# Performance work log

Hardware: AMD Instinct MI355X
Metric: run time of the kernel (lower is better)

Reference implementation:

```python
import jax, jax.numpy as jnp
import numpy as np

E = 1024   # n_embd
H = 16     # n_heads
D = 64     # head_dim
G = 4      # n_kv_groups
F = 4096   # ffn hidden_dim
V = 32000  # vocab
L = 4      # n_layers (all full_attention)
B = 1
T = 2048
ROT = 16   # partial_rotary_factor 0.25 * head_dim 64, rounded to even
EPS = 1e-6
THETA = 10000.0


def rope_tables(seq_len):
    # matches compute_rope_params: inv_freq over even indices of rotary_dim
    inv_freq = 1.0 / (THETA ** (jnp.arange(0, ROT, 2, dtype=jnp.float32) / ROT))
    ang = jnp.arange(seq_len, dtype=jnp.float32)[:, None] * inv_freq[None, :]
    ang = jnp.concatenate([ang, ang], axis=1)  # [T, ROT]
    return jnp.cos(ang), jnp.sin(ang)


def rmsnorm(x, w):
    # torch RMSNorm: x * rsqrt(mean(x^2)+eps) * (1 + weight)
    xf = x.astype(jnp.float32)
    n = xf * jax.lax.rsqrt(jnp.mean(xf * xf, axis=-1, keepdims=True) + EPS)
    return (n * (1.0 + w)).astype(x.dtype)


def apply_rope(x, cos, sin):
    # x: [B, h, T, D]; cos/sin: [1, 1, T, ROT]; partial rotary on first ROT dims
    x_rot, x_pass = x[..., :ROT], x[..., ROT:]
    x1, x2 = x_rot[..., :ROT // 2], x_rot[..., ROT // 2:]
    rotated = jnp.concatenate([-x2, x1], axis=-1)
    return jnp.concatenate([x_rot * cos + rotated * sin, x_pass], axis=-1)


def _forward(tokens, emb, Wq, Wk, Wv, Wo, qn, kn, n1, n2, f1, f2, f3, fn, head):
    cos, sin = rope_tables(T)
    cos = cos[None, None]  # [1,1,T,ROT]
    sin = sin[None, None]
    mask = jnp.triu(jnp.ones((T, T), dtype=bool), k=1)  # True = masked
    scale = D ** -0.5
    x = emb[tokens]  # [B,T,E]

    def block(x, p):
        wq, wk, wv, wo, qw, kw, w1, w2, g1, g2, g3 = p
        h = rmsnorm(x, w1)
        # fused Q + gate projection -> [B,T,H,2D], chunk on last dim
        qg = (h @ wq).reshape(B, T, H, 2 * D)
        q = qg[..., :D].transpose(0, 2, 1, 3)            # [B,H,T,D]
        gate = qg[..., D:].reshape(B, T, H * D)          # [B,T,H*D]
        k = (h @ wk).reshape(B, T, G, D).transpose(0, 2, 1, 3)  # [B,G,T,D]
        v = (h @ wv).reshape(B, T, G, D).transpose(0, 2, 1, 3)
        q = rmsnorm(q, qw)
        k = rmsnorm(k, kw)
        q = apply_rope(q, cos, sin)
        k = apply_rope(k, cos, sin)
        k = jnp.repeat(k, H // G, axis=1)  # GQA expand -> [B,H,T,D]
        v = jnp.repeat(v, H // G, axis=1)
        scores = jnp.einsum('bhqd,bhkd->bhqk', q, k)
        scores = jnp.where(mask, -jnp.inf, scores) * scale
        w = jax.nn.softmax(scores.astype(jnp.float32), axis=-1).astype(q.dtype)
        ctx = jnp.einsum('bhqk,bhkd->bhqd', w, v)
        ctx = ctx.transpose(0, 2, 1, 3).reshape(B, T, H * D)
        ctx = ctx * jax.nn.sigmoid(gate)
        x = x + ctx @ wo
        h2 = rmsnorm(x, w2)
        ff = (jax.nn.silu(h2 @ g1) * (h2 @ g2)) @ g3
        return x + ff, None

    params = (Wq, Wk, Wv, Wo, qn, kn, n1, n2, f1, f2, f3)
    x, _ = jax.lax.scan(block, x, params)
    return rmsnorm(x, fn) @ head  # logits [B,T,V]


def setup_inputs() -> dict:
    key = jax.random.key(0)
    ks = jax.random.split(key, 16)
    s = 0.02
    rn = lambda k, shape, sc=s: jax.random.normal(k, shape, jnp.float32) * sc
    return {
        'tokens': jax.random.randint(ks[0], (B, T), 0, V),
        'emb': rn(ks[1], (V, E)),
        'Wq': rn(ks[2], (L, E, 2 * H * D)),
        'Wk': rn(ks[3], (L, E, G * D)),
        'Wv': rn(ks[4], (L, E, G * D)),
        'Wo': rn(ks[5], (L, H * D, E)),
        'qn': rn(ks[6], (L, D)),
        'kn': rn(ks[7], (L, D)),
        'n1': rn(ks[8], (L, E)),
        'n2': rn(ks[9], (L, E)),
        'f1': rn(ks[10], (L, E, F)),
        'f2': rn(ks[11], (L, E, F)),
        'f3': rn(ks[12], (L, F, E)),
        'fn': rn(ks[13], (E,)),
        'head': rn(ks[14], (E, V)),
    }


def reference(tokens, emb, Wq, Wk, Wv, Wo, qn, kn, n1, n2, f1, f2, f3, fn, head):
    return _forward(tokens, emb, Wq, Wk, Wv, Wo, qn, kn, n1, n2, f1, f2, f3, fn, head)
```

## Files before the change

kernel.cpp:

```cpp
#include <hip/hip_runtime.h>

#define T_LEN 2048
#define E_DIM 1024
#define H_N 16
#define G_N 4
#define D_H 64
#define F_DIM 4096
#define V_SZ 32000
#define L_N 4

typedef __attribute__((ext_vector_type(8))) __bf16 bf16x8;
typedef __attribute__((ext_vector_type(4))) float f32x4;

__device__ __forceinline__ unsigned short f2bf(float f){
  unsigned int u = __float_as_uint(f);
  unsigned int r = (u + 0x7FFFu + ((u >> 16) & 1u)) >> 16;
  return (unsigned short)r;
}

__device__ __forceinline__ unsigned int packbf(float a, float b){
  return (unsigned int)f2bf(a) | ((unsigned int)f2bf(b) << 16);
}

__device__ __forceinline__ f32x4 mfma16(bf16x8 a, bf16x8 b, f32x4 c){
  return __builtin_amdgcn_mfma_f32_16x16x32_bf16(a, b, c, 0, 0, 0);
}

__device__ __forceinline__ void gl16(const void* g, void* l){
  __builtin_amdgcn_global_load_lds((const __attribute__((address_space(1))) void*)g,
                                   (__attribute__((address_space(3))) void*)l, 16, 0, 0);
}

#define SBAR() __builtin_amdgcn_s_barrier()
#define LGK0() do{ asm volatile("s_waitcnt lgkmcnt(0)" ::: "memory"); __builtin_amdgcn_sched_barrier(0); }while(0)
#define VMC4() do{ asm volatile("s_waitcnt vmcnt(4)" ::: "memory"); __builtin_amdgcn_sched_barrier(0); }while(0)
#define VMC0() do{ asm volatile("s_waitcnt vmcnt(0)" ::: "memory"); __builtin_amdgcn_sched_barrier(0); }while(0)

#define QSCALE 0.1803368801111183f

__global__ __launch_bounds__(256) void embed_k(const float* __restrict__ emb,
                                               const int* __restrict__ tokens,
                                               float* __restrict__ x){
  int t = blockIdx.x;
  int tok = tokens[t];
  const float4* src = (const float4*)(emb + (size_t)tok * E_DIM);
  float4* dst = (float4*)(x + (size_t)t * E_DIM);
  dst[threadIdx.x] = src[threadIdx.x];
}

__global__ __launch_bounds__(256) void transpose_bf16(const float* __restrict__ src,
                                                      unsigned short* __restrict__ dst,
                                                      int R, int C){
  __shared__ float tile[32][33];
  int c0 = blockIdx.x * 32, r0 = blockIdx.y * 32;
  int tx = threadIdx.x & 31, ty = threadIdx.x >> 5;
  for (int i = 0; i < 4; i++){
    int r = ty + i * 8;
    tile[r][tx] = src[(size_t)(r0 + r) * C + c0 + tx];
  }
  __syncthreads();
  for (int i = 0; i < 4; i++){
    int r = ty + i * 8;
    dst[(size_t)(c0 + r) * R + r0 + tx] = f2bf(tile[tx][r]);
  }
}

__device__ __forceinline__ void tr32(const float* __restrict__ src, unsigned short* __restrict__ dst,
                                     int R, int C, int bx, int by, float* tile ){
  int c0 = bx * 32, r0 = by * 32;
  int tx = threadIdx.x & 31, ty = threadIdx.x >> 5;
  for (int i = 0; i < 4; i++){
    int r = ty + i * 8;
    tile[r * 33 + tx] = src[(size_t)(r0 + r) * C + c0 + tx];
  }
  __syncthreads();
  for (int i = 0; i < 4; i++){
    int r = ty + i * 8;
    dst[(size_t)(c0 + r) * R + r0 + tx] = f2bf(tile[tx * 33 + r]);
  }
}

__global__ __launch_bounds__(256) void prep_weights(const float* __restrict__ Wq, const float* __restrict__ Wk,
                                                    const float* __restrict__ Wv, const float* __restrict__ Wo,
                                                    const float* __restrict__ f1, const float* __restrict__ f2,
                                                    const float* __restrict__ f3,
                                                    unsigned short* __restrict__ wt_qkv,
                                                    unsigned short* __restrict__ wt_o,
                                                    unsigned short* __restrict__ wt_f12i,
                                                    unsigned short* __restrict__ wt_f3){
  __shared__ float sh[1100];
  int id = blockIdx.x;
  if (id < 2048){ tr32(Wq, wt_qkv, 1024, 2048, id & 63, id >> 6, sh); return; }
  id -= 2048;
  if (id < 256){ tr32(Wk, wt_qkv + 2048 * 1024, 1024, 256, id & 7, id >> 3, sh); return; }
  id -= 256;
  if (id < 256){ tr32(Wv, wt_qkv + 2304 * 1024, 1024, 256, id & 7, id >> 3, sh); return; }
  id -= 256;
  if (id < 1024){ tr32(Wo, wt_o, 1024, 1024, id & 31, id >> 5, sh); return; }
  id -= 1024;
  if (id < 4096){ tr32(f3, wt_f3, 4096, 1024, id & 31, id >> 5, sh); return; }
  id -= 4096;
  {
    int q = id & 255, kb = id >> 8;
    float* t1 = sh; float* t2 = sh + 32 * 17;
    int c = threadIdx.x & 15, kk0 = threadIdx.x >> 4;
    for (int p = 0; p < 2; p++){
      int kk = p * 16 + kk0;
      t1[kk * 17 + c] = f1[(size_t)(kb * 32 + kk) * F_DIM + q * 16 + c];
      t2[kk * 17 + c] = f2[(size_t)(kb * 32 + kk) * F_DIM + q * 16 + c];
    }
    __syncthreads();
    int kk = threadIdx.x & 31, rb = threadIdx.x >> 5;
    for (int i = 0; i < 4; i++){
      int r = i * 8 + rb;
      float v = (r < 16) ? t1[kk * 17 + r] : t2[kk * 17 + (r - 16)];
      wt_f12i[(size_t)(q * 32 + r) * 1024 + kb * 32 + kk] = f2bf(v);
    }
  }
}

__global__ __launch_bounds__(256) void rmsnorm_k(const float* __restrict__ x,
                                                 const float* __restrict__ w,
                                                 unsigned short* __restrict__ out){
  const int t = blockIdx.x, tid = threadIdx.x;
  const float4 v = ((const float4*)(x + (size_t)t * E_DIM))[tid];
  float ss = v.x*v.x + v.y*v.y + v.z*v.z + v.w*v.w;
  for (int m = 1; m < 64; m <<= 1) ss += __shfl_xor(ss, m);
  __shared__ float red[4];
  if ((tid & 63) == 0) red[tid >> 6] = ss;
  __syncthreads();
  ss = red[0] + red[1] + red[2] + red[3];
  const float r = rsqrtf(ss * (1.0f / E_DIM) + 1e-6f);
  const float4 wv = ((const float4*)w)[tid];
  ushort4 o;
  o.x = f2bf(v.x * r * (1.0f + wv.x));
  o.y = f2bf(v.y * r * (1.0f + wv.y));
  o.z = f2bf(v.z * r * (1.0f + wv.z));
  o.w = f2bf(v.w * r * (1.0f + wv.w));
  ((ushort4*)(out + (size_t)t * E_DIM))[tid] = o;
}

template<int MODE>
__global__ __launch_bounds__(256) void gemm64_bt(const unsigned short* __restrict__ A,
                                                 const unsigned short* __restrict__ Bt,
                                                 float* __restrict__ C,
                                                 int M, int N, int K){
  __shared__ unsigned short As[64 * 32];
  __shared__ unsigned short Bs[128 * 32];
  const int tid = threadIdx.x;
  const int lane = tid & 63, w = tid >> 6;
  const int l15 = lane & 15, l4 = lane >> 4;

  const int chunk = gridDim.x >> 3;
  const int wgid = (blockIdx.x & 7) * chunk + (blockIdx.x >> 3);
  const int nm = M >> 6;
  const int bm = wgid % nm, bn = wgid / nm;
  const int m0 = bm * 64, n0 = bn * 128;

  const int KS = K / gridDim.y;
  const int kbeg = blockIdx.y * KS;

  const int r0 = tid >> 2;
  const int c0 = (tid & 3) << 3;

  const unsigned short* gA  = A  + (size_t)(m0 + r0) * K + c0;
  const unsigned short* gB0 = Bt + (size_t)(n0 + r0) * K + c0;
  const unsigned short* gB1 = Bt + (size_t)(n0 + 64 + r0) * K + c0;
  unsigned short* lA  = As + w * 512;
  unsigned short* lB0 = Bs + w * 512;
  unsigned short* lB1 = Bs + 2048 + w * 512;

  f32x4 acc[4][2] = {};

  for (int k0 = kbeg; k0 < kbeg + KS; k0 += 32){
    __syncthreads();
    gl16(gA  + k0, lA);
    gl16(gB0 + k0, lB0);
    gl16(gB1 + k0, lB1);
    __syncthreads();
    bf16x8 af[4], bfr[2];
    for (int i = 0; i < 4; i++)
      af[i] = *(const bf16x8*)&As[(i * 16 + l15) * 32 + l4 * 8];
    for (int j = 0; j < 2; j++)
      bfr[j] = *(const bf16x8*)&Bs[(w * 32 + j * 16 + l15) * 32 + l4 * 8];
    for (int i = 0; i < 4; i++)
      for (int j = 0; j < 2; j++)
        acc[i][j] = mfma16(af[i], bfr[j], acc[i][j]);
  }

  for (int i = 0; i < 4; i++)
    for (int j = 0; j < 2; j++){
      int col = n0 + w * 32 + j * 16 + l15;
      for (int r = 0; r < 4; r++){
        int row = m0 + i * 16 + l4 * 4 + r;
        size_t idx = (size_t)row * N + col;
        if (MODE == 0) C[idx] = acc[i][j][r];
        else if (MODE == 1) C[idx] += acc[i][j][r];
        else atomicAdd(&C[idx], acc[i][j][r]);
      }
    }
}

template<int EPI>
__global__ __launch_bounds__(512, 2) void gemm256(const unsigned short* __restrict__ A,
                                                  const unsigned short* __restrict__ Bt,
                                                  float* __restrict__ outF,
                                                  unsigned short* __restrict__ outH,
                                                  int M, int N, int K){
  __shared__ unsigned short lds[65536];
  const int tid = threadIdx.x;
  const int lane = tid & 63, w = tid >> 6;
  const int wm = w >> 2, wn = w & 3;
  const int l15 = lane & 15, l4 = lane >> 4;

  const int nwg = gridDim.x;
  const int xcd = (int)blockIdx.x & 7, lin = (int)blockIdx.x >> 3;
  const int q8 = nwg >> 3, r8 = nwg & 7;
  const int wgid = (xcd < r8 ? xcd * (q8 + 1) : r8 * (q8 + 1) + (xcd - r8) * q8) + lin;
  const int nm = M >> 8;
  const int bm = wgid % nm, bn = wgid / nm;
  const int m0 = bm * 256, n0 = bn * 256;

  const int KS = K / gridDim.y;
  const int kbeg = blockIdx.y * KS;
  const int NT = KS >> 6;

  const int srow = (lane >> 3);
  const int scol = lane & 7;

  auto stageA = [&](int b, int h, int kt){
    #pragma unroll
    for (int c = 0; c < 2; c++){
      int r = w * 16 + c * 8 + srow;
      const unsigned short* g = A + (size_t)(m0 + h * 128 + r) * K + kbeg + kt * 64 + ((scol ^ (r & 7)) << 3);
      gl16(g, (char*)lds + (b * 2 + h) * 16384 + (w * 16 + c * 8) * 128);
    }
  };
  auto stageB = [&](int b, int h, int kt){
    #pragma unroll
    for (int c = 0; c < 2; c++){
      int r = w * 16 + c * 8 + srow;
      const unsigned short* g = Bt + (size_t)(n0 + h * 128 + r) * K + kbeg + kt * 64 + ((scol ^ (r & 7)) << 3);
      gl16(g, (char*)lds + 65536 + (b * 2 + h) * 16384 + (w * 16 + c * 8) * 128);
    }
  };

  const int sl0 = ((l4)     ^ (l15 & 7)) << 4;
  const int sl1 = ((4 | l4) ^ (l15 & 7)) << 4;

  f32x4 acc[8][4] = {};
  bf16x8 aF[8], bF[8];

  stageA(0, 0, 0); stageA(0, 1, 0); stageB(0, 0, 0); stageB(0, 1, 0);
  if (NT > 1){ stageB(1, 0, 1); stageB(1, 1, 1); }
  VMC4();
  SBAR();

  for (int kt = 0; kt < NT; kt++){
    const int buf = kt & 1;
    const char* Ab = (const char*)lds + (buf * 2 + wm) * 16384;
    const char* Bb = (const char*)lds + 65536 + (buf * 2 + (wn >> 1)) * 16384;
    const int brbase = (wn & 1) * 64;

    #pragma unroll
    for (int mf = 0; mf < 4; mf++){
      int r = mf * 16 + l15;
      aF[mf * 2 + 0] = *(const bf16x8*)(Ab + r * 128 + sl0);
      aF[mf * 2 + 1] = *(const bf16x8*)(Ab + r * 128 + sl1);
    }
    #pragma unroll
    for (int nf = 0; nf < 2; nf++){
      int r = brbase + nf * 16 + l15;
      bF[nf * 2 + 0] = *(const bf16x8*)(Bb + r * 128 + sl0);
      bF[nf * 2 + 1] = *(const bf16x8*)(Bb + r * 128 + sl1);
    }
    if (kt + 1 < NT) stageA(buf ^ 1, 0, kt + 1);
    SBAR(); LGK0();
    __builtin_amdgcn_s_setprio(1);
    #pragma unroll
    for (int mf = 0; mf < 4; mf++)
      #pragma unroll
      for (int nf = 0; nf < 2; nf++){
        acc[mf][nf] = mfma16(aF[mf * 2 + 0], bF[nf * 2 + 0], acc[mf][nf]);
        acc[mf][nf] = mfma16(aF[mf * 2 + 1], bF[nf * 2 + 1], acc[mf][nf]);
      }
    __builtin_amdgcn_s_setprio(0);
    SBAR();

    #pragma unroll
    for (int nf = 2; nf < 4; nf++){
      int r = brbase + nf * 16 + l15;
      bF[nf * 2 + 0] = *(const bf16x8*)(Bb + r * 128 + sl0);
      bF[nf * 2 + 1] = *(const bf16x8*)(Bb + r * 128 + sl1);
    }
    if (kt + 1 < NT) stageA(buf ^ 1, 1, kt + 1);
    SBAR(); LGK0();
    __builtin_amdgcn_s_setprio(1);
    #pragma unroll
    for (int mf = 0; mf < 4; mf++)
      #pragma unroll
      for (int nf = 2; nf < 4; nf++){
        acc[mf][nf] = mfma16(aF[mf * 2 + 0], bF[nf * 2 + 0], acc[mf][nf]);
        acc[mf][nf] = mfma16(aF[mf * 2 + 1], bF[nf * 2 + 1], acc[mf][nf]);
      }
    __builtin_amdgcn_s_setprio(0);
    SBAR();

    #pragma unroll
    for (int mf = 0; mf < 4; mf++){
      int r = 64 + mf * 16 + l15;
      aF[mf * 2 + 0] = *(const bf16x8*)(Ab + r * 128 + sl0);
      aF[mf * 2 + 1] = *(const bf16x8*)(Ab + r * 128 + sl1);
    }
    if (kt + 2 < NT) stageB(buf, 0, kt + 2);
    SBAR(); LGK0();
    __builtin_amdgcn_s_setprio(1);
    #pragma unroll
    for (int mf = 0; mf < 4; mf++)
      #pragma unroll
      for (int nf = 2; nf < 4; nf++){
        acc[4 + mf][nf] = mfma16(aF[mf * 2 + 0], bF[nf * 2 + 0], acc[4 + mf][nf]);
        acc[4 + mf][nf] = mfma16(aF[mf * 2 + 1], bF[nf * 2 + 1], acc[4 + mf][nf]);
      }
    __builtin_amdgcn_s_setprio(0);
    SBAR();

    if (kt + 2 < NT) stageB(buf, 1, kt + 2);
    SBAR();
    __builtin_amdgcn_s_setprio(1);
    #pragma unroll
    for (int mf = 0; mf < 4; mf++)
      #pragma unroll
      for (int nf = 0; nf < 2; nf++){
        acc[4 + mf][nf] = mfma16(aF[mf * 2 + 0], bF[nf * 2 + 0], acc[4 + mf][nf]);
        acc[4 + mf][nf] = mfma16(aF[mf * 2 + 1], bF[nf * 2 + 1], acc[4 + mf][nf]);
      }
    __builtin_amdgcn_s_setprio(0);
    if (kt + 2 < NT) { VMC4(); } else { VMC0(); }
    SBAR();
  }

  if (EPI == 0 || EPI == 2){
    #pragma unroll
    for (int mfg = 0; mfg < 8; mfg++){
      #pragma unroll
      for (int nf = 0; nf < 4; nf++){
        int col = n0 + wn * 64 + nf * 16 + l15;
        int row0 = m0 + wm * 128 + mfg * 16 + l4 * 4;
        #pragma unroll
        for (int r = 0; r < 4; r++){
          size_t idx = (size_t)(row0 + r) * N + col;
          if (EPI == 0) outF[idx] = acc[mfg][nf][r];
          else atomicAdd(&outF[idx], acc[mfg][nf][r]);
        }
      }
    }
  } else {
    const int NH = N >> 1;
    #pragma unroll
    for (int mfg = 0; mfg < 8; mfg++){
      #pragma unroll
      for (int nfp = 0; nfp < 2; nfp++){
        int col = (n0 >> 1) + wn * 32 + nfp * 16 + l15;
        int row0 = m0 + wm * 128 + mfg * 16 + l4 * 4;
        #pragma unroll
        for (int r = 0; r < 4; r++){
          float u = acc[mfg][nfp * 2 + 0][r];
          float g = acc[mfg][nfp * 2 + 1][r];
          outH[(size_t)(row0 + r) * NH + col] = f2bf(u / (1.0f + __expf(-u)) * g);
        }
      }
    }
  }
}

__global__ __launch_bounds__(256) void qkvpost_k(const float* __restrict__ qkv,
                                                 const float* __restrict__ qn,
                                                 const float* __restrict__ kn,
                                                 unsigned short* __restrict__ qb,
                                                 unsigned short* __restrict__ kb,
                                                 unsigned short* __restrict__ vt){
  const int t = blockIdx.x;
  const int lane = threadIdx.x & 63, w = threadIdx.x >> 6;
  const int d = lane;
  const int fi = d & 7;
  const float invf = powf(10000.0f, -(float)fi * 0.125f);
  const float ang = (float)t * invf;
  const float c = cosf(ang), s = sinf(ang);

  for (int i = 0; i < 4; i++){
    int h = w * 4 + i;
    float v = qkv[(size_t)t * 2560 + h * 128 + d];
    float ss = v * v;
    for (int m = 1; m < 64; m <<= 1) ss += __shfl_xor(ss, m);
    float r = rsqrtf(ss * (1.0f / D_H) + 1e-6f);
    float xn = v * r * (1.0f + qn[d]);
    float partner = __shfl_xor(xn, 8);
    float o;
    if (d < 8)       o = xn * c - partner * s;
    else if (d < 16) o = xn * c + partner * s;
    else             o = xn;
    qb[((size_t)h * T_LEN + t) * D_H + d] = f2bf(o * QSCALE);
  }
  {
    float v = qkv[(size_t)t * 2560 + 2048 + w * 64 + d];
    float ss = v * v;
    for (int m = 1; m < 64; m <<= 1) ss += __shfl_xor(ss, m);
    float r = rsqrtf(ss * (1.0f / D_H) + 1e-6f);
    float xn = v * r * (1.0f + kn[d]);
    float partner = __shfl_xor(xn, 8);
    float o;
    if (d < 8)       o = xn * c - partner * s;
    else if (d < 16) o = xn * c + partner * s;
    else             o = xn;
    kb[((size_t)w * T_LEN + t) * D_H + d] = f2bf(o);
  }
  {
    float v = qkv[(size_t)t * 2560 + 2304 + w * 64 + d];
    vt[((size_t)(w * 64 + d)) * T_LEN + t] = f2bf(v);
  }
}

__global__ __launch_bounds__(256) void attn_k(const unsigned short* __restrict__ qb,
                                              const unsigned short* __restrict__ kb,
                                              const unsigned short* __restrict__ vt,
                                              const float* __restrict__ qkv,
                                              unsigned short* __restrict__ ctxg){
  const int qt = blockIdx.x, h = blockIdx.y;
  const int g = h >> 2;
  const int tid = threadIdx.x;
  const int wv = tid >> 6;
  const int lane = tid & 63;
  const int l15 = lane & 15, l4 = lane >> 4;
  const int q0 = qt * 16;
  const int nch = (q0 >> 6) + 1;

  __shared__ unsigned short Pl[4][16][72];
  __shared__ float sO[4][16][66];
  __shared__ float sM[4][16];
  __shared__ float sL[4][16];

  const bf16x8 aq0 = *(const bf16x8*)(qb + ((size_t)h * T_LEN + q0 + l15) * D_H + l4 * 8);
  const bf16x8 aq1 = *(const bf16x8*)(qb + ((size_t)h * T_LEN + q0 + l15) * D_H + 32 + l4 * 8);

  f32x4 acc[4] = {};
  float m = -1e30f, lpart = 0.0f;

  for (int c = wv; c < nch; c += 4){
    const int kv0 = c << 6;
    f32x4 sc[4];
    #pragma unroll
    for (int cp = 0; cp < 4; cp++){
      const unsigned short* kbase = kb + ((size_t)g * T_LEN + kv0 + cp * 16 + l15) * D_H + l4 * 8;
      bf16x8 bk0 = *(const bf16x8*)(kbase);
      bf16x8 bk1 = *(const bf16x8*)(kbase + 32);
      f32x4 z = {0.f, 0.f, 0.f, 0.f};
      z = mfma16(bk0, aq0, z);
      z = mfma16(bk1, aq1, z);
      sc[cp] = z;
    }
    if (c == nch - 1){
      #pragma unroll
      for (int cp = 0; cp < 4; cp++)
        #pragma unroll
        for (int j = 0; j < 4; j++){
          int kv = kv0 + cp * 16 + l4 * 4 + j;
          sc[cp][j] = (kv <= q0 + l15) ? sc[cp][j] : -1e30f;
        }
    }
    float mx = sc[0][0];
    #pragma unroll
    for (int cp = 0; cp < 4; cp++)
      #pragma unroll
      for (int j = 0; j < 4; j++) mx = fmaxf(mx, sc[cp][j]);
    mx = fmaxf(mx, __shfl_xor(mx, 16));
    mx = fmaxf(mx, __shfl_xor(mx, 32));
    const float mnew = fmaxf(m, mx);
    const bool grew = !__all(mnew == m);
    const float mold = m;
    m = mnew;

    float ssum = 0.0f;
    unsigned int up[4][2];
    #pragma unroll
    for (int cp = 0; cp < 4; cp++){
      float p0 = exp2f(sc[cp][0] - mnew);
      float p1 = exp2f(sc[cp][1] - mnew);
      float p2 = exp2f(sc[cp][2] - mnew);
      float p3 = exp2f(sc[cp][3] - mnew);
      ssum += (p0 + p1) + (p2 + p3);
      up[cp][0] = packbf(p0, p1);
      up[cp][1] = packbf(p2, p3);
    }
    if (grew){
      const float resc = exp2f(mold - mnew);
      lpart *= resc;
      float r0 = __shfl(resc, l4 * 4 + 0);
      float r1 = __shfl(resc, l4 * 4 + 1);
      float r2 = __shfl(resc, l4 * 4 + 2);
      float r3 = __shfl(resc, l4 * 4 + 3);
      #pragma unroll
      for (int nt = 0; nt < 4; nt++){
        acc[nt][0] *= r0; acc[nt][1] *= r1; acc[nt][2] *= r2; acc[nt][3] *= r3;
      }
    }
    lpart += ssum;

    #pragma unroll
    for (int cp = 0; cp < 4; cp++){
      uint2 pr; pr.x = up[cp][0]; pr.y = up[cp][1];
      *(uint2*)&Pl[wv][l15][cp * 16 + l4 * 4] = pr;
    }
    asm volatile("s_waitcnt lgkmcnt(0)" ::: "memory");
    const bf16x8 pa0 = *(const bf16x8*)&Pl[wv][l15][l4 * 8];
    const bf16x8 pa1 = *(const bf16x8*)&Pl[wv][l15][32 + l4 * 8];
    #pragma unroll
    for (int nt = 0; nt < 4; nt++){
      const unsigned short* vbase = vt + ((size_t)g * 64 + nt * 16 + l15) * T_LEN + kv0;
      bf16x8 bv0 = *(const bf16x8*)(vbase + l4 * 8);
      bf16x8 bv1 = *(const bf16x8*)(vbase + 32 + l4 * 8);
      acc[nt] = mfma16(pa1, bv1, mfma16(pa0, bv0, acc[nt]));
    }
  }

  lpart += __shfl_xor(lpart, 16);
  lpart += __shfl_xor(lpart, 32);

  #pragma unroll
  for (int j = 0; j < 4; j++){
    int row = l4 * 4 + j;
    #pragma unroll
    for (int nt = 0; nt < 4; nt++)
      sO[wv][row][nt * 16 + l15] = acc[nt][j];
  }
  if (l4 == 0){
    sM[wv][l15] = m;
    sL[wv][l15] = lpart;
  }
  __syncthreads();

  #pragma unroll
  for (int rr = 0; rr < 4; rr++){
    int r = wv * 4 + rr;
    float m0 = sM[0][r], m1 = sM[1][r], m2 = sM[2][r], m3 = sM[3][r];
    float ms = fmaxf(fmaxf(m0, m1), fmaxf(m2, m3));
    float w0 = exp2f(m0 - ms), w1 = exp2f(m1 - ms), w2 = exp2f(m2 - ms), w3 = exp2f(m3 - ms);
    float accv = w0 * sO[0][r][lane] + w1 * sO[1][r][lane] + w2 * sO[2][r][lane] + w3 * sO[3][r][lane];
    float lsum = w0 * sL[0][r] + w1 * sL[1][r] + w2 * sL[2][r] + w3 * sL[3][r];
    float gate = qkv[(size_t)(q0 + r) * 2560 + h * 128 + 64 + lane];
    float val = accv / lsum * (1.0f / (1.0f + __expf(-gate)));
    ctxg[(size_t)(q0 + r) * (H_N * D_H) + h * D_H + lane] = f2bf(val);
  }
}

extern "C" void kernel_launch(void* const* d_in, const int* in_sizes, int n_in,
                              void* d_out, int out_size, void* d_ws, size_t ws_size,
                              hipStream_t stream){
  (void)in_sizes; (void)n_in; (void)out_size; (void)ws_size;
  const int*   tokens = (const int*)d_in[0];
  const float* emb    = (const float*)d_in[1];
  const float* Wq     = (const float*)d_in[2];
  const float* Wk     = (const float*)d_in[3];
  const float* Wv     = (const float*)d_in[4];
  const float* Wo     = (const float*)d_in[5];
  const float* qn     = (const float*)d_in[6];
  const float* kn     = (const float*)d_in[7];
  const float* n1     = (const float*)d_in[8];
  const float* n2     = (const float*)d_in[9];
  const float* f1     = (const float*)d_in[10];
  const float* f2     = (const float*)d_in[11];
  const float* f3     = (const float*)d_in[12];
  const float* fn     = (const float*)d_in[13];
  const float* head   = (const float*)d_in[14];
  float* out = (float*)d_out;

  char* ws = (char*)d_ws;
  size_t off = 0;
  auto alloc = [&](size_t bytes)->char*{
    char* p = ws + off;
    off += (bytes + 255) & ~(size_t)255;
    return p;
  };
  float*          x       = (float*)alloc((size_t)T_LEN * E_DIM * 4);
  unsigned short* hbf     = (unsigned short*)alloc((size_t)T_LEN * E_DIM * 2);
  float*          qkvf    = (float*)alloc((size_t)T_LEN * 2560 * 4);
  unsigned short* qb      = (unsigned short*)alloc((size_t)H_N * T_LEN * D_H * 2);
  unsigned short* kb      = (unsigned short*)alloc((size_t)G_N * T_LEN * D_H * 2);
  unsigned short* vt      = (unsigned short*)alloc((size_t)G_N * D_H * T_LEN * 2);
  unsigned short* ctxg    = (unsigned short*)alloc((size_t)T_LEN * E_DIM * 2);
  unsigned short* hg      = (unsigned short*)alloc((size_t)T_LEN * F_DIM * 2);
  unsigned short* wt_qkv  = (unsigned short*)alloc((size_t)2560 * E_DIM * 2);
  unsigned short* wt_o    = (unsigned short*)alloc((size_t)E_DIM * E_DIM * 2);
  unsigned short* wt_f12i = (unsigned short*)alloc((size_t)2 * F_DIM * E_DIM * 2);
  unsigned short* wt_f3   = (unsigned short*)alloc((size_t)E_DIM * F_DIM * 2);
  unsigned short* wt_head = (unsigned short*)alloc((size_t)V_SZ * E_DIM * 2);

  embed_k<<<T_LEN, 256, 0, stream>>>(emb, tokens, x);
  transpose_bf16<<<dim3(V_SZ / 32, E_DIM / 32), 256, 0, stream>>>(head, wt_head, E_DIM, V_SZ);

  for (int l = 0; l < L_N; l++){
    prep_weights<<<15872, 256, 0, stream>>>(Wq + (size_t)l * E_DIM * 2048,
                                            Wk + (size_t)l * E_DIM * 256,
                                            Wv + (size_t)l * E_DIM * 256,
                                            Wo + (size_t)l * E_DIM * E_DIM,
                                            f1 + (size_t)l * E_DIM * F_DIM,
                                            f2 + (size_t)l * E_DIM * F_DIM,
                                            f3 + (size_t)l * F_DIM * E_DIM,
                                            wt_qkv, wt_o, wt_f12i, wt_f3);

    rmsnorm_k<<<T_LEN, 256, 0, stream>>>(x, n1 + l * E_DIM, hbf);
    gemm64_bt<0><<<(T_LEN / 64) * (2560 / 128), 256, 0, stream>>>(hbf, wt_qkv, qkvf, T_LEN, 2560, E_DIM);
    qkvpost_k<<<T_LEN, 256, 0, stream>>>(qkvf, qn + l * D_H, kn + l * D_H, qb, kb, vt);
    attn_k<<<dim3(T_LEN / 16, H_N), 256, 0, stream>>>(qb, kb, vt, qkvf, ctxg);
    gemm64_bt<2><<<dim3((T_LEN / 64) * (E_DIM / 128), 2), 256, 0, stream>>>(ctxg, wt_o, x, T_LEN, E_DIM, E_DIM);

    rmsnorm_k<<<T_LEN, 256, 0, stream>>>(x, n2 + l * E_DIM, hbf);
    gemm256<1><<<(T_LEN / 256) * (2 * F_DIM / 256), 512, 0, stream>>>(hbf, wt_f12i, nullptr, hg, T_LEN, 2 * F_DIM, E_DIM);
    gemm256<2><<<dim3((T_LEN / 256) * (E_DIM / 256), 8), 512, 0, stream>>>(hg, wt_f3, x, nullptr, T_LEN, E_DIM, F_DIM);
  }

  rmsnorm_k<<<T_LEN, 256, 0, stream>>>(x, fn, hbf);
  gemm256<0><<<(T_LEN / 256) * (V_SZ / 256), 512, 0, stream>>>(hbf, wt_head, out, nullptr, T_LEN, V_SZ, E_DIM);
}
```

Measured before the change: 1.386 ms.

## Replace small QKV/O GEMM with 128x256 double-buffered swizzled MFMA kernel

```diff
diff --git a/kernel.cpp b/kernel.cpp
--- a/kernel.cpp
+++ b/kernel.cpp
@@ -141,62 +141,129 @@
 }
 
 template<int MODE>
-__global__ __launch_bounds__(256) void gemm64_bt(const unsigned short* __restrict__ A,
-                                                 const unsigned short* __restrict__ Bt,
-                                                 float* __restrict__ C,
-                                                 int M, int N, int K){
-  __shared__ unsigned short As[64 * 32];
-  __shared__ unsigned short Bs[128 * 32];
+__global__ __launch_bounds__(512) void gemm128(const unsigned short* __restrict__ A,
+                                               const unsigned short* __restrict__ Bt,
+                                               float* __restrict__ C,
+                                               int M, int N, int K){
+  __shared__ unsigned short lds[49152];
   const int tid = threadIdx.x;
   const int lane = tid & 63, w = tid >> 6;
+  const int wm = w >> 2, wn = w & 3;
   const int l15 = lane & 15, l4 = lane >> 4;
 
-  const int chunk = gridDim.x >> 3;
-  const int wgid = (blockIdx.x & 7) * chunk + (blockIdx.x >> 3);
-  const int nm = M >> 6;
+  const int nwg = gridDim.x;
+  const int xcd = (int)blockIdx.x & 7, lin = (int)blockIdx.x >> 3;
+  const int q8 = nwg >> 3, r8 = nwg & 7;
+  const int wgid = (xcd < r8 ? xcd * (q8 + 1) : r8 * (q8 + 1) + (xcd - r8) * q8) + lin;
+  const int nm = M >> 7;
   const int bm = wgid % nm, bn = wgid / nm;
-  const int m0 = bm * 64, n0 = bn * 128;
+  const int m0 = bm * 128, n0 = bn * 256;
 
   const int KS = K / gridDim.y;
   const int kbeg = blockIdx.y * KS;
-
-  const int r0 = tid >> 2;
-  const int c0 = (tid & 3) << 3;
-
-  const unsigned short* gA  = A  + (size_t)(m0 + r0) * K + c0;
-  const unsigned short* gB0 = Bt + (size_t)(n0 + r0) * K + c0;
-  const unsigned short* gB1 = Bt + (size_t)(n0 + 64 + r0) * K + c0;
-  unsigned short* lA  = As + w * 512;
-  unsigned short* lB0 = Bs + w * 512;
-  unsigned short* lB1 = Bs + 2048 + w * 512;
-
-  f32x4 acc[4][2] = {};
-
-  for (int k0 = kbeg; k0 < kbeg + KS; k0 += 32){
-    __syncthreads();
-    gl16(gA  + k0, lA);
-    gl16(gB0 + k0, lB0);
-    gl16(gB1 + k0, lB1);
-    __syncthreads();
-    bf16x8 af[4], bfr[2];
-    for (int i = 0; i < 4; i++)
-      af[i] = *(const bf16x8*)&As[(i * 16 + l15) * 32 + l4 * 8];
-    for (int j = 0; j < 2; j++)
-      bfr[j] = *(const bf16x8*)&Bs[(w * 32 + j * 16 + l15) * 32 + l4 * 8];
-    for (int i = 0; i < 4; i++)
-      for (int j = 0; j < 2; j++)
-        acc[i][j] = mfma16(af[i], bfr[j], acc[i][j]);
-  }
-
-  for (int i = 0; i < 4; i++)
-    for (int j = 0; j < 2; j++){
-      int col = n0 + w * 32 + j * 16 + l15;
+  const int NT = KS >> 6;
+
+  const int srow = (lane >> 3);
+  const int scol = lane & 7;
+
+  auto stageA = [&](int b, int kt){
+    #pragma unroll
+    for (int c = 0; c < 2; c++){
+      int r = w * 16 + c * 8 + srow;
+      const unsigned short* g = A + (size_t)(m0 + r) * K + kbeg + kt * 64 + ((scol ^ (r & 7)) << 3);
+      gl16(g, (char*)lds + b * 16384 + (w * 16 + c * 8) * 128);
+    }
+  };
+  auto stageB = [&](int b, int h, int kt){
+    #pragma unroll
+    for (int c = 0; c < 2; c++){
+      int r = w * 16 + c * 8 + srow;
+      const unsigned short* g = Bt + (size_t)(n0 + h * 128 + r) * K + kbeg + kt * 64 + ((scol ^ (r & 7)) << 3);
+      gl16(g, (char*)lds + 32768 + (b * 2 + h) * 16384 + (w * 16 + c * 8) * 128);
+    }
+  };
+
+  const int sl0 = ((l4)     ^ (l15 & 7)) << 4;
+  const int sl1 = ((4 | l4) ^ (l15 & 7)) << 4;
+
+  f32x4 acc[4][4] = {};
+  bf16x8 aF[8], bF[8];
+
+  stageA(0, 0); stageB(0, 0, 0); stageB(0, 1, 0);
+  if (NT > 1){ stageB(1, 0, 1); stageB(1, 1, 1); }
+  VMC4();
+  SBAR();
+
+  for (int kt = 0; kt < NT; kt++){
+    const int buf = kt & 1;
+    const char* Ab = (const char*)lds + buf * 16384;
+    const char* Bb = (const char*)lds + 32768 + (buf * 2 + (wn >> 1)) * 16384;
+    const int brbase = (wn & 1) * 64;
+
+    #pragma unroll
+    for (int mf = 0; mf < 4; mf++){
+      int r = wm * 64 + mf * 16 + l15;
+      aF[mf * 2 + 0] = *(const bf16x8*)(Ab + r * 128 + sl0);
+      aF[mf * 2 + 1] = *(const bf16x8*)(Ab + r * 128 + sl1);
+    }
+    #pragma unroll
+    for (int nf = 0; nf < 2; nf++){
+      int r = brbase + nf * 16 + l15;
+      bF[nf * 2 + 0] = *(const bf16x8*)(Bb + r * 128 + sl0);
+      bF[nf * 2 + 1] = *(const bf16x8*)(Bb + r * 128 + sl1);
+    }
+    if (kt + 1 < NT) stageA(buf ^ 1, kt + 1);
+    SBAR(); LGK0();
+    __builtin_amdgcn_s_setprio(1);
+    #pragma unroll
+    for (int mf = 0; mf < 4; mf++)
+      #pragma unroll
+      for (int nf = 0; nf < 2; nf++){
+        acc[mf][nf] = mfma16(aF[mf * 2 + 0], bF[nf * 2 + 0], acc[mf][nf]);
+        acc[mf][nf] = mfma16(aF[mf * 2 + 1], bF[nf * 2 + 1], acc[mf][nf]);
+      }
+    __builtin_amdgcn_s_setprio(0);
+    SBAR();
+
+    #pragma unroll
+    for (int nf = 2; nf < 4; nf++){
+      int r = brbase + nf * 16 + l15;
+      bF[nf * 2 + 0] = *(const bf16x8*)(Bb + r * 128 + sl0);
+      bF[nf * 2 + 1] = *(const bf16x8*)(Bb + r * 128 + sl1);
+    }
+    SBAR(); LGK0();
+    __builtin_amdgcn_s_setprio(1);
+    #pragma unroll
+    for (int mf = 0; mf < 4; mf++)
+      #pragma unroll
+      for (int nf = 2; nf < 4; nf++){
+        acc[mf][nf] = mfma16(aF[mf * 2 + 0], bF[nf * 2 + 0], acc[mf][nf]);
+        acc[mf][nf] = mfma16(aF[mf * 2 + 1], bF[nf * 2 + 1], acc[mf][nf]);
+      }
+    __builtin_amdgcn_s_setprio(0);
+    SBAR();
+
+    if (kt + 2 < NT){
+      stageB(buf, 0, kt + 2);
+      stageB(buf, 1, kt + 2);
+      VMC4();
+    } else {
+      VMC0();
+    }
+    SBAR();
+  }
+
+  #pragma unroll
+  for (int mf = 0; mf < 4; mf++)
+    #pragma unroll
+    for (int nf = 0; nf < 4; nf++){
+      int col = n0 + wn * 64 + nf * 16 + l15;
+      int row0 = m0 + wm * 64 + mf * 16 + l4 * 4;
+      #pragma unroll
       for (int r = 0; r < 4; r++){
-        int row = m0 + i * 16 + l4 * 4 + r;
-        size_t idx = (size_t)row * N + col;
-        if (MODE == 0) C[idx] = acc[i][j][r];
-        else if (MODE == 1) C[idx] += acc[i][j][r];
-        else atomicAdd(&C[idx], acc[i][j][r]);
+        size_t idx = (size_t)(row0 + r) * N + col;
+        if (MODE == 0) C[idx] = acc[mf][nf][r];
+        else atomicAdd(&C[idx], acc[mf][nf][r]);
       }
     }
 }
@@ -609,10 +676,10 @@
                                             wt_qkv, wt_o, wt_f12i, wt_f3);
 
     rmsnorm_k<<<T_LEN, 256, 0, stream>>>(x, n1 + l * E_DIM, hbf);
-    gemm64_bt<0><<<(T_LEN / 64) * (2560 / 128), 256, 0, stream>>>(hbf, wt_qkv, qkvf, T_LEN, 2560, E_DIM);
+    gemm128<0><<<(T_LEN / 128) * (2560 / 256), 512, 0, stream>>>(hbf, wt_qkv, qkvf, T_LEN, 2560, E_DIM);
     qkvpost_k<<<T_LEN, 256, 0, stream>>>(qkvf, qn + l * D_H, kn + l * D_H, qb, kb, vt);
     attn_k<<<dim3(T_LEN / 16, H_N), 256, 0, stream>>>(qb, kb, vt, qkvf, ctxg);
-    gemm64_bt<2><<<dim3((T_LEN / 64) * (E_DIM / 128), 2), 256, 0, stream>>>(ctxg, wt_o, x, T_LEN, E_DIM, E_DIM);
+    gemm128<2><<<dim3((T_LEN / 128) * (E_DIM / 256), 4), 512, 0, stream>>>(ctxg, wt_o, x, T_LEN, E_DIM, E_DIM);
 
     rmsnorm_k<<<T_LEN, 256, 0, stream>>>(x, n2 + l * E_DIM, hbf);
     gemm256<1><<<(T_LEN / 256) * (2 * F_DIM / 256), 512, 0, stream>>>(hbf, wt_f12i, nullptr, hg, T_LEN, 2 * F_DIM, E_DIM);
```

Measured after the change: 1.396 ms. No clear change (+0.7%).
